# Kernel optimization log

Measured on AMD Instinct MI355X. Metric: run time of the kernel, lower is better.

## Reference

```python
import jax, jax.numpy as jnp
import numpy as np
from jax import lax

N_HEADS = 12
HEAD_DIM = 64
ALPHA = 4.0  # spikingjelly surrogate.Sigmoid default alpha
EPS = 1e-5   # BatchNorm1d default eps

@jax.custom_vjp
def _heaviside(v):
    return (v >= 0.0).astype(v.dtype)

def _heaviside_fwd(v):
    return _heaviside(v), v

def _heaviside_bwd(v, g):
    sg = jax.nn.sigmoid(ALPHA * v)
    return (g * ALPHA * sg * (1.0 - sg),)

_heaviside.defvjp(_heaviside_fwd, _heaviside_bwd)

def if_node(x):
    """Multi-step IFNode (v_threshold=1, hard reset to 0), scan over leading T dim."""
    def step(v, xt):
        v = v + xt                      # integrate
        s = _heaviside(v - 1.0)         # fire
        v = (1.0 - s) * v               # hard reset: spiked neurons -> 0
        return v, s
    _, spikes = lax.scan(step, jnp.zeros_like(x[0]), x)
    return spikes

def bn1d(x):
    """Fresh (training-mode) BatchNorm1d over (T, S, D) with channels=S;
    affine weight=1, bias=0 at init, so pure normalization over axes (0,2)."""
    mean = x.mean(axis=(0, 2), keepdims=True)
    var = x.var(axis=(0, 2), keepdims=True)  # biased variance, as torch BN uses
    return (x - mean) * lax.rsqrt(var + EPS)

def setup_inputs() -> dict:
    key = jax.random.key(0)
    ks = jax.random.split(key, 5)
    T, S, D = 4, 2048, 768
    x = jax.random.normal(ks[0], (T, S, D), dtype=jnp.float32)
    scale = 0.02
    wq = jax.random.normal(ks[1], (D, D), dtype=jnp.float32) * scale
    wk = jax.random.normal(ks[2], (D, D), dtype=jnp.float32) * scale
    wv = jax.random.normal(ks[3], (D, D), dtype=jnp.float32) * scale
    wo = jax.random.normal(ks[4], (D, D), dtype=jnp.float32) * scale
    return {"x": x, "wq": wq, "wk": wk, "wv": wv, "wo": wo, "cur_pos": S}

def reference(x, wq, wk, wv, wo, cur_pos):
    T, S, D = x.shape
    tmp = if_node(x)                    # init_spike
    Q = tmp @ wq
    V = tmp @ wv
    K = tmp @ wk
    Q = if_node(bn1d(Q))                # spike_q(bnq(Q))
    V = if_node(bn1d(V))                # spike_v(bnv(V))
    K = if_node(bn1d(K))                # spike_k(bnk(K))
    # (T, S, H, hd) -> (T, H, S, hd)
    Qh = Q.reshape(T, S, N_HEADS, HEAD_DIM).transpose(0, 2, 1, 3)
    Vh = V.reshape(T, S, N_HEADS, HEAD_DIM).transpose(0, 2, 1, 3)
    Kh = K.reshape(T, S, N_HEADS, HEAD_DIM).transpose(0, 2, 1, 3)
    QK = (Qh * Kh).sum(axis=2, keepdims=True)   # (T, H, 1, hd)
    QK = if_node(QK)                    # talking_heads
    QKV = Vh * QK                       # (T, H, S, hd)
    QKV = QKV.transpose(0, 2, 1, 3).reshape(T, S, D)
    return bn1d(QKV @ wo)
```

## Files before the change

### kernel.cpp

```cpp
#include <hip/hip_runtime.h>

#define T_ 4
#define S_ 2048
#define D_ 768
#define SD_ (S_ * D_)
#define TSD_ (T_ * SD_)
#define H_ 12
#define HD_ 64
#define PLANE_BYTES 2359296u

typedef int int32x4 __attribute__((ext_vector_type(4)));

__device__ __forceinline__ void cp16(unsigned char* lds, const unsigned char* g) {
    __builtin_amdgcn_global_load_lds(
        (const __attribute__((address_space(1))) unsigned int*)g,
        (__attribute__((address_space(3))) unsigned int*)lds, 16, 0, 0);
}

__device__ __forceinline__ size_t frag_addr(int m, int d) {
    return ((size_t)(m >> 4) * 12 + (d >> 6)) * 1024 +
           (size_t)(((d >> 4) & 3) * 256 + (m & 15) * 16 + (d & 15));
}

__global__ __launch_bounds__(256) void k_prep_all(const float* __restrict__ wq,
                                                  const float* __restrict__ wk,
                                                  const float* __restrict__ wv,
                                                  const float* __restrict__ wo,
                                                  const float* __restrict__ x,
                                                  unsigned char* __restrict__ Bp,
                                                  unsigned char* __restrict__ Sx) {
    if (blockIdx.y < 4) {
        const float* W = (blockIdx.y == 0) ? wq : (blockIdx.y == 1) ? wk
                       : (blockIdx.y == 2) ? wv : wo;
        unsigned char* out = Bp + (size_t)blockIdx.y * PLANE_BYTES;
        int idx = blockIdx.x * 256 + threadIdx.x;
        int j0 = idx & 3;
        int lane = (idx >> 2) & 63;
        int kb = (idx >> 8) % 12;
        int rest = (idx >> 8) / 12;
        int nbg = rest % 48;
        int p = rest / 48;
        int n = nbg * 16 + (lane & 15);
        int kbase = kb * 64 + (lane >> 4) * 16 + j0 * 4;
        unsigned int packed = 0;
#pragma unroll
        for (int jj = 0; jj < 4; jj++) {
            float w = W[(size_t)(kbase + jj) * D_ + n];
            int u = (int)rintf(w * 1073741824.0f);
            for (int i = 0; i < p; i++) u = (u + 128) >> 8;
            packed |= ((unsigned int)(u & 255)) << (8 * jj);
        }
        *(unsigned int*)(out + (size_t)idx * 4) = packed;
    } else {
        int i = blockIdx.x * 256 + threadIdx.x;
        int idx = i * 4;
        if (idx >= SD_) return;
        int s = idx / D_;
        int d = idx % D_;
        double v[4] = {0.0, 0.0, 0.0, 0.0};
#pragma unroll
        for (int t = 0; t < T_; t++) {
            float4 xt = *(const float4*)(x + (size_t)t * SD_ + idx);
            float xs[4] = {xt.x, xt.y, xt.z, xt.w};
            uchar4 sp;
            unsigned char* so = &sp.x;
#pragma unroll
            for (int j = 0; j < 4; j++) {
                v[j] += (double)xs[j];
                unsigned char ss = (v[j] >= 1.0) ? 1 : 0;
                so[j] = ss;
                if (ss) v[j] = 0.0;
            }
            *(uchar4*)(Sx + frag_addr(t * S_ + s, d)) = sp;
        }
    }
}

#define LDSBUF 16384

__global__ __launch_bounds__(256, 3) void k_gemm_i8(
    const unsigned char* __restrict__ A,
    const unsigned char* __restrict__ Bp,
    const unsigned char* __restrict__ Ms,
    float* __restrict__ C0, float* __restrict__ C1, float* __restrict__ C2,
    int bzoff) {
    int z = blockIdx.z;
    const unsigned char* B = Bp + (size_t)(bzoff + z) * PLANE_BYTES;
    float* C = (z == 0) ? C0 : (z == 1) ? C1 : C2;

    __shared__ __align__(16) unsigned char smem[2 * LDSBUF];

    int tid = threadIdx.x;
    int lane = tid & 63;
    int w = tid >> 6;
    int wm = w >> 1;
    int wn = w & 1;
    int row0 = blockIdx.x * 64;
    int tI = row0 >> 11;
    int n0 = blockIdx.y * 64;
    int nbg0 = blockIdx.y * 4;
    int col = lane & 15;
    int quad = lane >> 4;

    int32x4 zerov = {0, 0, 0, 0};
    int32x4 acc[2][2][4];
#pragma unroll
    for (int mb = 0; mb < 2; mb++)
#pragma unroll
        for (int nb = 0; nb < 2; nb++)
#pragma unroll
            for (int p = 0; p < 4; p++) acc[mb][nb][p] = zerov;

    const unsigned char* Abase =
        A + ((size_t)((row0 >> 4) + wm * 2) * 12) * 1024 + lane * 16;

    auto stage = [&](int buf, int kb) {
        unsigned char* bb = smem + buf * LDSBUF;
#pragma unroll
        for (int qi = 0; qi < 4; qi++) {
            int q = 4 * w + qi;
            int p = q >> 2, nb = q & 3;
            cp16(bb + q * 1024,
                 B + (size_t)((p * 48 + nbg0 + nb) * 12 + kb) * 1024 + lane * 16);
        }
    };

    int32x4 a_cur[2], a_nxt[2];
    a_cur[0] = *(const int32x4*)(Abase);
    a_cur[1] = *(const int32x4*)(Abase + 12288);
    stage(0, 0);
    __syncthreads();

    for (int kb = 0; kb < 12; kb++) {
        int cur = kb & 1;
        if (kb < 11) {
            stage(1 - cur, kb + 1);
            a_nxt[0] = *(const int32x4*)(Abase + (kb + 1) * 1024);
            a_nxt[1] = *(const int32x4*)(Abase + 12288 + (kb + 1) * 1024);
        }
        int32x4 af0 = a_cur[0], af1 = a_cur[1];
        if (Ms) {
            int32x4 mv = *(const int32x4*)(Ms + tI * D_ + kb * 64 + quad * 16);
            af0 &= mv;
            af1 &= mv;
        }
        const unsigned char* bb = smem + cur * LDSBUF;
#pragma unroll
        for (int p = 0; p < 4; p++)
#pragma unroll
            for (int nb = 0; nb < 2; nb++) {
                int32x4 bf = *(const int32x4*)(
                    bb + (size_t)(p * 4 + wn * 2 + nb) * 1024 + lane * 16);
                acc[0][nb][p] = __builtin_amdgcn_mfma_i32_16x16x64_i8(
                    af0, bf, acc[0][nb][p], 0, 0, 0);
                acc[1][nb][p] = __builtin_amdgcn_mfma_i32_16x16x64_i8(
                    af1, bf, acc[1][nb][p], 0, 0, 0);
            }
        __syncthreads();
        a_cur[0] = a_nxt[0];
        a_cur[1] = a_nxt[1];
    }

#pragma unroll
    for (int mb = 0; mb < 2; mb++)
#pragma unroll
        for (int nb = 0; nb < 2; nb++)
#pragma unroll
            for (int r = 0; r < 4; r++) {
                long t = (long)acc[mb][nb][0][r] + ((long)acc[mb][nb][1][r] << 8)
                       + ((long)acc[mb][nb][2][r] << 16)
                       + ((long)acc[mb][nb][3][r] << 24);
                float v = (float)((double)t * (1.0 / 1073741824.0));
                int rr = row0 + wm * 32 + mb * 16 + quad * 4 + r;
                int cc = n0 + wn * 32 + nb * 16 + col;
                C[(size_t)rr * D_ + cc] = v;
            }
}

__global__ __launch_bounds__(256) void k_bn_if(const float* __restrict__ Qf,
                                               const float* __restrict__ Kf,
                                               const float* __restrict__ Vf,
                                               unsigned char* __restrict__ Qs,
                                               unsigned char* __restrict__ Ks,
                                               unsigned char* __restrict__ Vs) {
    int s = blockIdx.x;
    int y = blockIdx.y;
    const float* X = (y == 0) ? Qf : (y == 1) ? Kf : Vf;
    unsigned char* Sp = (y == 0) ? Qs : (y == 1) ? Ks : Vs;

    __shared__ float buf[T_][D_];
    __shared__ double red[16];

    int tid = threadIdx.x;
    double sum = 0.0, sumsq = 0.0;
#pragma unroll
    for (int t = 0; t < T_; t++) {
        for (int d = tid; d < D_; d += 256) {
            float v = X[(size_t)t * SD_ + (size_t)s * D_ + d];
            buf[t][d] = v;
            double dv = (double)v;
            sum += dv;
            sumsq += dv * dv;
        }
    }
#pragma unroll
    for (int off = 32; off > 0; off >>= 1) {
        sum += __shfl_down(sum, off);
        sumsq += __shfl_down(sumsq, off);
    }
    int lane = tid & 63, wv = tid >> 6;
    if (lane == 0) { red[wv] = sum; red[4 + wv] = sumsq; }
    __syncthreads();
    if (tid == 0) {
        double s4 = red[0] + red[1] + red[2] + red[3];
        double q4 = red[4] + red[5] + red[6] + red[7];
        double mean = s4 / 3072.0;
        double var = q4 / 3072.0 - mean * mean;
        red[8] = mean;
        red[9] = 1.0 / sqrt(var + 1e-5);
    }
    __syncthreads();
    double mean = red[8], rstd = red[9];
    for (int d = tid; d < D_; d += 256) {
        double v = 0.0;
#pragma unroll
        for (int t = 0; t < T_; t++) {
            double xn = ((double)buf[t][d] - mean) * rstd;
            v += xn;
            int sp = (v >= 1.0) ? 1 : 0;
            Sp[frag_addr(t * S_ + s, d)] = (unsigned char)sp;
            if (sp) v = 0.0;
        }
    }
}

__global__ __launch_bounds__(256) void k_qk(const unsigned char* __restrict__ Qs,
                                            const unsigned char* __restrict__ Ks,
                                            float* __restrict__ QK) {
    int t = blockIdx.x / H_;
    int h = blockIdx.x % H_;
    int lane = threadIdx.x & 63;
    int w = threadIdx.x >> 6;
    size_t base = ((size_t)t * 128 * 12 + h) * 1024 + lane * 16;
    uint4 acc = make_uint4(0, 0, 0, 0);
    for (int c = w; c < 128; c += 4) {
        uint4 q = *(const uint4*)(Qs + base + (size_t)c * 12288);
        uint4 k = *(const uint4*)(Ks + base + (size_t)c * 12288);
        acc.x += q.x & k.x;
        acc.y += q.y & k.y;
        acc.z += q.z & k.z;
        acc.w += q.w & k.w;
    }
    __shared__ unsigned int part[4][64][4];
    part[w][lane][0] = acc.x;
    part[w][lane][1] = acc.y;
    part[w][lane][2] = acc.z;
    part[w][lane][3] = acc.w;
    __syncthreads();
    if (threadIdx.x < 64) {
        int quad = threadIdx.x >> 4;
        int rem = threadIdx.x & 15;
        int dw = rem >> 2;
        int b = rem & 3;
        unsigned int tot = 0;
#pragma unroll
        for (int ww = 0; ww < 4; ww++)
            for (int cc = 0; cc < 16; cc++)
                tot += (part[ww][quad * 16 + cc][dw] >> (8 * b)) & 255u;
        QK[t * D_ + h * HD_ + quad * 16 + dw * 4 + b] = (float)tot;
    }
}

__global__ __launch_bounds__(256) void k_if_qk(const float* __restrict__ QK,
                                               unsigned char* __restrict__ QKm) {
    int j = blockIdx.x * 256 + threadIdx.x;
    if (j >= D_) return;
    float v = 0.f;
#pragma unroll
    for (int t = 0; t < T_; t++) {
        v += QK[t * D_ + j];
        unsigned char sp = (v >= 1.0f) ? 1 : 0;
        QKm[t * D_ + j] = sp;
        if (sp) v = 0.f;
    }
}

__global__ __launch_bounds__(256) void k_bn_out(const float* __restrict__ Xin,
                                                float* __restrict__ out) {
    int s = blockIdx.x;
    __shared__ float buf[T_][D_];
    __shared__ double red[16];
    int tid = threadIdx.x;
    double sum = 0.0, sumsq = 0.0;
#pragma unroll
    for (int t = 0; t < T_; t++) {
        for (int d = tid; d < D_; d += 256) {
            float v = Xin[(size_t)t * SD_ + (size_t)s * D_ + d];
            buf[t][d] = v;
            double dv = (double)v;
            sum += dv;
            sumsq += dv * dv;
        }
    }
#pragma unroll
    for (int off = 32; off > 0; off >>= 1) {
        sum += __shfl_down(sum, off);
        sumsq += __shfl_down(sumsq, off);
    }
    int lane = tid & 63, wv = tid >> 6;
    if (lane == 0) { red[wv] = sum; red[4 + wv] = sumsq; }
    __syncthreads();
    if (tid == 0) {
        double s4 = red[0] + red[1] + red[2] + red[3];
        double q4 = red[4] + red[5] + red[6] + red[7];
        double mean = s4 / 3072.0;
        double var = q4 / 3072.0 - mean * mean;
        red[8] = mean;
        red[9] = 1.0 / sqrt(var + 1e-5);
    }
    __syncthreads();
    double mean = red[8], rstd = red[9];
    for (int d = tid; d < D_; d += 256) {
#pragma unroll
        for (int t = 0; t < T_; t++) {
            double v = (double)buf[t][d];
            out[(size_t)t * SD_ + (size_t)s * D_ + d] =
                (float)((v - mean) * rstd);
        }
    }
}

extern "C" void kernel_launch(void* const* d_in, const int* in_sizes, int n_in,
                              void* d_out, int out_size, void* d_ws,
                              size_t ws_size, hipStream_t stream) {
    const float* x  = (const float*)d_in[0];
    const float* wq = (const float*)d_in[1];
    const float* wk = (const float*)d_in[2];
    const float* wv = (const float*)d_in[3];
    const float* wo = (const float*)d_in[4];
    float* out = (float*)d_out;

    float* ws  = (float*)d_ws;
    float* Qf  = ws;
    float* Kf  = ws + (size_t)TSD_;
    float* Vf  = ws + (size_t)2 * TSD_;
    float* QK  = ws + (size_t)3 * TSD_;
    unsigned char* QKm = (unsigned char*)(QK + T_ * D_);
    unsigned char* Sx  = QKm + 4096;
    unsigned char* Ks  = Sx + (size_t)TSD_;
    unsigned char* Vs  = Ks + (size_t)TSD_;
    unsigned char* Bp  = Vs + (size_t)TSD_;
    unsigned char* Qs  = Sx;

    k_prep_all<<<dim3(589824 / 256, 5), 256, 0, stream>>>(wq, wk, wv, wo, x,
                                                          Bp, Sx);
    k_gemm_i8<<<dim3(128, 12, 3), 256, 0, stream>>>(Sx, Bp, nullptr,
                                                    Qf, Kf, Vf, 0);
    k_bn_if<<<dim3(S_, 3), 256, 0, stream>>>(Qf, Kf, Vf, Qs, Ks, Vs);
    k_qk<<<T_ * H_, 256, 0, stream>>>(Qs, Ks, QK);
    k_if_qk<<<3, 256, 0, stream>>>(QK, QKm);
    k_gemm_i8<<<dim3(128, 12, 1), 256, 0, stream>>>(Vs, Bp, QKm, Qf, Qf, Qf, 3);
    k_bn_out<<<S_, 256, 0, stream>>>(Qf, out);
}
```

Before: 239.1 us.

## Drop LDS staging in int8 GEMM, load B fragments directly to registers

The int8 MFMA GEMM no longer stages B tiles into LDS with global_load_lds and no longer synchronises per k-block. Each wave now loads its own A and B fragments straight from global memory into double-buffered registers. The block M tile doubles to 128 rows, so each wave computes 64x32 and the grid halves. This removes LDS traffic and barriers but increases register pressure (occupancy hint lowered to 2) and loses B sharing across waves, relying on L2/cache for reuse.

```diff
diff --git a/kernel.cpp b/kernel.cpp
--- a/kernel.cpp
+++ b/kernel.cpp
@@ -10,12 +10,6 @@
 #define PLANE_BYTES 2359296u
 
 typedef int int32x4 __attribute__((ext_vector_type(4)));
-
-__device__ __forceinline__ void cp16(unsigned char* lds, const unsigned char* g) {
-    __builtin_amdgcn_global_load_lds(
-        (const __attribute__((address_space(1))) unsigned int*)g,
-        (__attribute__((address_space(3))) unsigned int*)lds, 16, 0, 0);
-}
 
 __device__ __forceinline__ size_t frag_addr(int m, int d) {
     return ((size_t)(m >> 4) * 12 + (d >> 6)) * 1024 +
@@ -76,9 +70,7 @@
     }
 }
 
-#define LDSBUF 16384
-
-__global__ __launch_bounds__(256, 3) void k_gemm_i8(
+__global__ __launch_bounds__(256, 2) void k_gemm_i8(
     const unsigned char* __restrict__ A,
     const unsigned char* __restrict__ Bp,
     const unsigned char* __restrict__ Ms,
@@ -88,81 +80,77 @@
     const unsigned char* B = Bp + (size_t)(bzoff + z) * PLANE_BYTES;
     float* C = (z == 0) ? C0 : (z == 1) ? C1 : C2;
 
-    __shared__ __align__(16) unsigned char smem[2 * LDSBUF];
-
     int tid = threadIdx.x;
     int lane = tid & 63;
     int w = tid >> 6;
     int wm = w >> 1;
     int wn = w & 1;
-    int row0 = blockIdx.x * 64;
+    int row0 = blockIdx.x * 128;
     int tI = row0 >> 11;
     int n0 = blockIdx.y * 64;
-    int nbg0 = blockIdx.y * 4;
+    int nbg0 = blockIdx.y * 4 + wn * 2;
     int col = lane & 15;
     int quad = lane >> 4;
 
     int32x4 zerov = {0, 0, 0, 0};
-    int32x4 acc[2][2][4];
-#pragma unroll
-    for (int mb = 0; mb < 2; mb++)
+    int32x4 acc[4][2][4];
+#pragma unroll
+    for (int mb = 0; mb < 4; mb++)
 #pragma unroll
         for (int nb = 0; nb < 2; nb++)
 #pragma unroll
             for (int p = 0; p < 4; p++) acc[mb][nb][p] = zerov;
 
-    const unsigned char* Abase =
-        A + ((size_t)((row0 >> 4) + wm * 2) * 12) * 1024 + lane * 16;
-
-    auto stage = [&](int buf, int kb) {
-        unsigned char* bb = smem + buf * LDSBUF;
-#pragma unroll
-        for (int qi = 0; qi < 4; qi++) {
-            int q = 4 * w + qi;
-            int p = q >> 2, nb = q & 3;
-            cp16(bb + q * 1024,
-                 B + (size_t)((p * 48 + nbg0 + nb) * 12 + kb) * 1024 + lane * 16);
-        }
-    };
-
-    int32x4 a_cur[2], a_nxt[2];
-    a_cur[0] = *(const int32x4*)(Abase);
-    a_cur[1] = *(const int32x4*)(Abase + 12288);
-    stage(0, 0);
-    __syncthreads();
+    const unsigned char* Ab =
+        A + ((size_t)((row0 >> 4) + wm * 4) * 12) * 1024 + lane * 16;
+    const unsigned char* Bb = B + lane * 16;
+
+    int32x4 a[2][4], b[2][8];
+#pragma unroll
+    for (int mb = 0; mb < 4; mb++)
+        a[0][mb] = *(const int32x4*)(Ab + (size_t)mb * 12288);
+#pragma unroll
+    for (int q = 0; q < 8; q++) {
+        int p = q >> 1, nb = q & 1;
+        b[0][q] = *(const int32x4*)(
+            Bb + (size_t)((p * 48 + nbg0 + nb) * 12) * 1024);
+    }
 
     for (int kb = 0; kb < 12; kb++) {
-        int cur = kb & 1;
-        if (kb < 11) {
-            stage(1 - cur, kb + 1);
-            a_nxt[0] = *(const int32x4*)(Abase + (kb + 1) * 1024);
-            a_nxt[1] = *(const int32x4*)(Abase + 12288 + (kb + 1) * 1024);
-        }
-        int32x4 af0 = a_cur[0], af1 = a_cur[1];
+        int cur = kb & 1, nxt = 1 - cur;
+        int kn = (kb < 11) ? kb + 1 : kb;
+#pragma unroll
+        for (int mb = 0; mb < 4; mb++)
+            a[nxt][mb] = *(const int32x4*)(
+                Ab + (size_t)mb * 12288 + (size_t)kn * 1024);
+#pragma unroll
+        for (int q = 0; q < 8; q++) {
+            int p = q >> 1, nb = q & 1;
+            b[nxt][q] = *(const int32x4*)(
+                Bb + (size_t)((p * 48 + nbg0 + nb) * 12 + kn) * 1024);
+        }
+        int32x4 af[4];
+#pragma unroll
+        for (int mb = 0; mb < 4; mb++) af[mb] = a[cur][mb];
         if (Ms) {
             int32x4 mv = *(const int32x4*)(Ms + tI * D_ + kb * 64 + quad * 16);
-            af0 &= mv;
-            af1 &= mv;
-        }
-        const unsigned char* bb = smem + cur * LDSBUF;
+#pragma unroll
+            for (int mb = 0; mb < 4; mb++) af[mb] &= mv;
+        }
 #pragma unroll
         for (int p = 0; p < 4; p++)
 #pragma unroll
             for (int nb = 0; nb < 2; nb++) {
-                int32x4 bf = *(const int32x4*)(
-                    bb + (size_t)(p * 4 + wn * 2 + nb) * 1024 + lane * 16);
-                acc[0][nb][p] = __builtin_amdgcn_mfma_i32_16x16x64_i8(
-                    af0, bf, acc[0][nb][p], 0, 0, 0);
-                acc[1][nb][p] = __builtin_amdgcn_mfma_i32_16x16x64_i8(
-                    af1, bf, acc[1][nb][p], 0, 0, 0);
+                int32x4 bf = b[cur][p * 2 + nb];
+#pragma unroll
+                for (int mb = 0; mb < 4; mb++)
+                    acc[mb][nb][p] = __builtin_amdgcn_mfma_i32_16x16x64_i8(
+                        af[mb], bf, acc[mb][nb][p], 0, 0, 0);
             }
-        __syncthreads();
-        a_cur[0] = a_nxt[0];
-        a_cur[1] = a_nxt[1];
-    }
-
-#pragma unroll
-    for (int mb = 0; mb < 2; mb++)
+    }
+
+#pragma unroll
+    for (int mb = 0; mb < 4; mb++)
 #pragma unroll
         for (int nb = 0; nb < 2; nb++)
 #pragma unroll
@@ -171,7 +159,7 @@
                        + ((long)acc[mb][nb][2][r] << 16)
                        + ((long)acc[mb][nb][3][r] << 24);
                 float v = (float)((double)t * (1.0 / 1073741824.0));
-                int rr = row0 + wm * 32 + mb * 16 + quad * 4 + r;
+                int rr = row0 + wm * 64 + mb * 16 + quad * 4 + r;
                 int cc = n0 + wn * 32 + nb * 16 + col;
                 C[(size_t)rr * D_ + cc] = v;
             }
@@ -354,11 +342,11 @@
 
     k_prep_all<<<dim3(589824 / 256, 5), 256, 0, stream>>>(wq, wk, wv, wo, x,
                                                           Bp, Sx);
-    k_gemm_i8<<<dim3(128, 12, 3), 256, 0, stream>>>(Sx, Bp, nullptr,
-                                                    Qf, Kf, Vf, 0);
+    k_gemm_i8<<<dim3(64, 12, 3), 256, 0, stream>>>(Sx, Bp, nullptr,
+                                                   Qf, Kf, Vf, 0);
     k_bn_if<<<dim3(S_, 3), 256, 0, stream>>>(Qf, Kf, Vf, Qs, Ks, Vs);
     k_qk<<<T_ * H_, 256, 0, stream>>>(Qs, Ks, QK);
     k_if_qk<<<3, 256, 0, stream>>>(QK, QKm);
-    k_gemm_i8<<<dim3(128, 12, 1), 256, 0, stream>>>(Vs, Bp, QKm, Qf, Qf, Qf, 3);
+    k_gemm_i8<<<dim3(64, 12, 1), 256, 0, stream>>>(Vs, Bp, QKm, Qf, Qf, Qf, 3);
     k_bn_out<<<S_, 256, 0, stream>>>(Qf, out);
 }
```

After: 278.7 us. +16.6%, slower.
